# Kernel optimization log

Measured on AMD Instinct MI355X. Metric: run time of the kernel, lower is better.

The kernel has to match this reference:

```python
import jax, jax.numpy as jnp
import numpy as np

# Module hyperparameters (from init_kwargs)
H, F = 8, 32            # num_heads, attention_filters
RY, RX = 3, 3           # spatial_radius
PH, PW = 2 * RY + 1, 2 * RX + 1
S = PH * PW             # patch_size = 49
HF = H * F


def setup_inputs() -> dict:
    key = jax.random.key(0)
    ks = jax.random.split(key, 6)
    B, Y, X, C = 4, 64, 64, 256
    x = jax.random.normal(ks[0], (B, Y, X, C), jnp.float32)
    # 1x1 conv kernels == dense matrices over the channel dim (no bias)
    Wq = jax.random.normal(ks[1], (C, HF), jnp.float32) / np.sqrt(C)
    Wk = jax.random.normal(ks[2], (C, HF), jnp.float32) / np.sqrt(C)
    Wv = jax.random.normal(ks[3], (C, HF), jnp.float32) / np.sqrt(C)
    Wo = jax.random.normal(ks[4], (HF, C), jnp.float32) / np.sqrt(HF)
    pos_emb = jax.random.normal(ks[5], (S, HF), jnp.float32) * 0.02
    return {"x": x, "Wq": Wq, "Wk": Wk, "Wv": Wv, "Wo": Wo, "pos_emb": pos_emb}


def reference(x, Wq, Wk, Wv, Wo, pos_emb):
    B, Y, X, C = x.shape
    dtype = x.dtype
    # 1x1 conv projections
    Q = x @ Wq                       # (B,Y,X,HF)
    K = x @ Wk
    V = x @ Wv
    # clipped patch centers (borders reuse interior patches)
    cy = jnp.clip(jnp.arange(Y), RY, Y - RY - 1)   # (Y,)
    cx = jnp.clip(jnp.arange(X), RX, X - RX - 1)   # (X,)
    # query relative-position indices within its patch
    qy = jnp.arange(Y) - cy + RY
    qx = jnp.arange(X) - cx + RX
    qidx = qy[:, None] * PW + qx[None, :]          # (Y,X) in [0,S)
    Q = Q + pos_emb[qidx]                          # add query pos embedding (HF)
    Q = Q.reshape(B, Y, X, H, F)
    K = K.reshape(B, Y, X, H, F)
    V = V.reshape(B, Y, X, H, F)
    cy_g, cx_g = jnp.meshgrid(cy, cx, indexing="ij")  # (Y,X)
    scale = jnp.asarray(1.0 / np.sqrt(F), dtype)
    NEG = jnp.asarray(-1e9, dtype)
    m = jnp.full((B, Y, X, H, 1), NEG, dtype)      # running max
    l = jnp.zeros((B, Y, X, H, 1), dtype)          # running sum-exp
    acc = jnp.zeros((B, Y, X, H, F), dtype)        # running value accumulator
    dy_vec = np.arange(-RY, RY + 1)                # within-chunk offsets ('col' mode)
    for dx in range(-RX, RX + 1):                  # chunk loop over columns (7 chunks)
        ny = jnp.clip(cy_g[None, :, :] + dy_vec[:, None, None], 0, Y - 1)  # (PH,Y,X)
        nx = jnp.clip(cx_g[None, :, :] + dx, 0, X - 1)                     # (1,Y,X)
        nx = jnp.broadcast_to(nx, ny.shape)
        sidx = (dy_vec + RY) * PW + (dx + RX)      # (PH,) relative-pos indices
        # gather neighbor K/V: (B,PH,Y,X,H,F)
        Kc = K[:, ny, nx] + pos_emb[sidx].reshape(PH, 1, 1, H, F)
        Vc = V[:, ny, nx]
        sc = jnp.einsum("byxhf,bsyxhf->byxhs", Q, Kc) * scale  # (B,Y,X,H,PH)
        new_m = jnp.maximum(m, sc.max(axis=-1, keepdims=True))
        alpha = jnp.exp(m - new_m)
        p = jnp.exp(sc - new_m)
        l = l * alpha + p.sum(axis=-1, keepdims=True)
        acc = acc * alpha + jnp.einsum("byxhs,bsyxhf->byxhf", p, Vc)
        m = new_m
    out = (acc / (l + 1e-8)).reshape(B, Y, X, HF) @ Wo
    return out
```

## Files before the change

### kernel.cpp

```cpp
#include <hip/hip_runtime.h>
#include <hip/hip_bf16.h>

static constexpr int NPOS = 4 * 64 * 64;
static constexpr int CD   = 256;
#define QSCALE (0.17677669529663687f * 1.4426950408889634f)

typedef __attribute__((ext_vector_type(8))) short bf16x8;
typedef __attribute__((ext_vector_type(4))) float f32x4;

__device__ __forceinline__ float bf2f(unsigned short u) {
    return __uint_as_float((unsigned int)u << 16);
}
__device__ __forceinline__ unsigned short bfbits(float f) {
    union { __hip_bfloat16 h; unsigned short u; } cv;
    cv.h = __float2bfloat16(f);
    return cv.u;
}
__device__ __forceinline__ unsigned int packbf2(float lo, float hi) {
    union { __hip_bfloat162 h; unsigned int u; } cv;
    cv.h.x = __float2bfloat16(lo);
    cv.h.y = __float2bfloat16(hi);
    return cv.u;
}
__device__ __forceinline__ uint4 pack8(float4 a, float4 b) {
    uint4 u;
    u.x = packbf2(a.x, a.y); u.y = packbf2(a.z, a.w);
    u.z = packbf2(b.x, b.y); u.w = packbf2(b.z, b.w);
    return u;
}
template<int CTRL>
__device__ __forceinline__ float dpp_mov(float v) {
    return __int_as_float(
        __builtin_amdgcn_update_dpp(0, __float_as_int(v), CTRL, 0xF, 0xF, true));
}
template<int IMM>
__device__ __forceinline__ float swz(float v) {
    return __int_as_float(__builtin_amdgcn_ds_swizzle(__float_as_int(v), IMM));
}

__global__ __launch_bounds__(256) void convert_kernel(
    const float* __restrict__ Wq, const float* __restrict__ Wk,
    const float* __restrict__ Wv, const float* __restrict__ Wo,
    const float* __restrict__ pe,
    __hip_bfloat16* __restrict__ Wfrag,
    __hip_bfloat16* __restrict__ pebf,
    __hip_bfloat16* __restrict__ Wofrag)
{
    int t = blockIdx.x * 256 + threadIdx.x;
    if (t < 24576) {
        int L = t & 63, ng = (t >> 6) & 7, s = (t >> 9) & 7, T = t >> 12;
        int mat = T >> 1;
        const float* src = (mat == 0) ? Wq : (mat == 1) ? Wk : Wv;
        int ncol  = (T & 1) * 128 + ng * 16 + (L & 15);
        int kbase = s * 32 + (L >> 4) * 8;
        __hip_bfloat16* dst = Wfrag + ((size_t)((T * 8 + s) * 8 + ng) * 64 + L) * 8;
#pragma unroll
        for (int j = 0; j < 8; ++j)
            dst[j] = __float2bfloat16(src[(kbase + j) * 256 + ncol]);
    } else if (t < 26624) {
        int u = t - 24576;
        int L = u & 63, Tn = (u >> 6) & 3, h = u >> 8;
        int s = Tn * 16 + (L & 15);
        int kbase = (L >> 4) * 8;
        __hip_bfloat16* dst = pebf + ((size_t)((h * 4 + Tn) * 64 + L)) * 8;
#pragma unroll
        for (int j = 0; j < 8; ++j) {
            float v = (s < 49) ? pe[s * 256 + h * 32 + kbase + j] * QSCALE : 0.f;
            dst[j] = __float2bfloat16(v);
        }
    } else if (t < 34816) {
        int u = t - 26624;
        int L = u & 63, ng = (u >> 6) & 7, s = (u >> 9) & 7, T = (u >> 12) & 1;
        int ncol  = T * 128 + ng * 16 + (L & 15);
        int kbase = s * 32 + (L >> 4) * 8;
        __hip_bfloat16* dst = Wofrag + ((size_t)((T * 8 + s) * 8 + ng) * 64 + L) * 8;
#pragma unroll
        for (int j = 0; j < 8; ++j)
            dst[j] = __float2bfloat16(Wo[(kbase + j) * 256 + ncol]);
    }
}

__global__ __launch_bounds__(256, 4) void qkv_mfma(
    const float* __restrict__ x,
    const __hip_bfloat16* __restrict__ Wfrag,
    const float* __restrict__ pe,
    unsigned short* __restrict__ QA,
    unsigned short* __restrict__ Kd,
    unsigned short* __restrict__ Vt)
{
    __shared__ __align__(16) unsigned short smem[256 * 68];
    short* As0 = (short*)smem;
    short* As1 = As0 + 2048;
    const int t = threadIdx.x;
    const int rowbase = blockIdx.x * 64;
    const int g = blockIdx.y;
    const int L = t & 63;
    const int wave = t >> 6;
    const int quad = L >> 4, lrow = L & 15;
    const int T = g * 2 + (wave >> 1);
    const int ngb = (wave & 1) * 4;

    f32x4 acc[4][4];
#pragma unroll
    for (int i = 0; i < 4; ++i)
#pragma unroll
        for (int j = 0; j < 4; ++j) acc[i][j] = (f32x4){0.f, 0.f, 0.f, 0.f};

    const float* xsrc = x + (size_t)(rowbase + (t >> 2)) * CD + (t & 3) * 8;
    const __hip_bfloat16* wbase = Wfrag + ((size_t)(T * 8 * 8 + ngb) * 64 + L) * 8;

    float4 f0 = ((const float4*)xsrc)[0];
    float4 f1 = ((const float4*)xsrc)[1];
    ((uint4*)As0)[t] = pack8(f0, f1);
    f0 = ((const float4*)(xsrc + 32))[0];
    f1 = ((const float4*)(xsrc + 32))[1];

    bf16x8 bfr[4];
#pragma unroll
    for (int j = 0; j < 4; ++j)
        bfr[j] = *(const bf16x8*)(wbase + (size_t)j * 64 * 8);
    __syncthreads();

#pragma unroll
    for (int s = 0; s < 8; ++s) {
        bf16x8 nbfr[4];
        if (s < 7) {
#pragma unroll
            for (int j = 0; j < 4; ++j)
                nbfr[j] = *(const bf16x8*)(wbase + (size_t)((s + 1) * 8 + j) * 64 * 8);
        }
        if (s < 7) {
            ((uint4*)((s & 1) ? As0 : As1))[t] = pack8(f0, f1);
            if (s < 6) {
                f0 = ((const float4*)(xsrc + (s + 2) * 32))[0];
                f1 = ((const float4*)(xsrc + (s + 2) * 32))[1];
            }
        }
        const short* Ab = (s & 1) ? As1 : As0;
#pragma unroll
        for (int i = 0; i < 4; ++i) {
            bf16x8 af = *(const bf16x8*)(Ab + (i * 16 + lrow) * 32 + quad * 8);
#pragma unroll
            for (int j = 0; j < 4; ++j)
                acc[i][j] = __builtin_amdgcn_mfma_f32_16x16x32_bf16(af, bfr[j], acc[i][j], 0, 0, 0);
        }
        __syncthreads();
#pragma unroll
        for (int j = 0; j < 4; ++j) bfr[j] = nbfr[j];
    }

    if (g == 0) {
#pragma unroll
        for (int i = 0; i < 4; ++i)
#pragma unroll
            for (int r = 0; r < 4; ++r) {
                int row = rowbase + i * 16 + quad * 4 + r;
                int yy = (row >> 6) & 63, xx = row & 63;
                int cy = min(max(yy, 3), 60), cx = min(max(xx, 3), 60);
                int qidx = (yy - cy + 3) * 7 + (xx - cx + 3);
#pragma unroll
                for (int j = 0; j < 4; ++j) {
                    int c = wave * 64 + j * 16 + lrow;
                    QA[(size_t)row * CD + c] = bfbits(acc[i][j][r] + pe[qidx * 256 + c]);
                }
            }
    } else if (g == 1) {
#pragma unroll
        for (int i = 0; i < 4; ++i)
#pragma unroll
            for (int r = 0; r < 4; ++r) {
                int row = rowbase + i * 16 + quad * 4 + r;
#pragma unroll
                for (int j = 0; j < 4; ++j) {
                    int c = wave * 64 + j * 16 + lrow;
                    Kd[(size_t)row * CD + c] = bfbits(acc[i][j][r] * QSCALE);
                }
            }
    } else {
        unsigned short* vt = smem;
#pragma unroll
        for (int i = 0; i < 4; ++i)
#pragma unroll
            for (int j = 0; j < 4; ++j) {
                int c = wave * 64 + j * 16 + lrow;
                int row0 = i * 16 + quad * 4;
                *(unsigned int*)&vt[c * 68 + row0] =
                    (unsigned int)bfbits(acc[i][j][0]) | ((unsigned int)bfbits(acc[i][j][1]) << 16);
                *(unsigned int*)&vt[c * 68 + row0 + 2] =
                    (unsigned int)bfbits(acc[i][j][2]) | ((unsigned int)bfbits(acc[i][j][3]) << 16);
            }
        __syncthreads();
        const int grp = t >> 4, lig = t & 15;
        const int row_off = lig * 4;
#pragma unroll
        for (int pass = 0; pass < 16; ++pass) {
            int c = pass * 16 + grp;
            *(ushort4*)(Vt + (size_t)c * 16384 + rowbase + row_off) =
                *(const ushort4*)&vt[c * 68 + row_off];
        }
    }
}

__global__ __launch_bounds__(512) void attn_oproj(
    const unsigned short* __restrict__ QA,
    const unsigned short* __restrict__ Kd,
    const unsigned short* __restrict__ Vt,
    const __hip_bfloat16* __restrict__ pebf,
    const __hip_bfloat16* __restrict__ Wofrag,
    float* __restrict__ out)
{
    __shared__ unsigned short qpes[8][16 * 64];
    __shared__ __align__(16) unsigned short ps[8][16 * 40];
    __shared__ __align__(16) unsigned short At[16 * 264];
    const int t = threadIdx.x, w = t >> 6, L = t & 63;
    const int lrow = L & 15, quad = L >> 4;
    const int pos0 = blockIdx.x * 16;
    const int x0 = pos0 & 63;
    const int yy = (pos0 >> 6) & 63, bb = pos0 >> 12;
    const int cy = min(max(yy, 3), 60);
    const int h = w;

    int cxr[4];
#pragma unroll
    for (int r = 0; r < 4; ++r)
        cxr[r] = min(max(x0 + quad * 4 + r, 3), 60) - x0 + 5;

    const int kc0 = min(max(x0 - 8 + lrow, 0), 63);
    const int kc1 = min(max(x0 + 8 + lrow, 0), 63);
    const f32x4 zero = {0.f, 0.f, 0.f, 0.f};
    unsigned short* qp = qpes[w];
    unsigned short* pw = ps[w];

    const bf16x8 qa = *(const bf16x8*)(QA + (size_t)(pos0 + lrow) * 256 + h * 32 + quad * 8);

#pragma unroll
    for (int Tn = 0; Tn < 4; ++Tn) {
        bf16x8 bp = *(const bf16x8*)(pebf + ((size_t)((h * 4 + Tn) * 64 + L)) * 8);
        f32x4 c = __builtin_amdgcn_mfma_f32_16x16x32_bf16(qa, bp, zero, 0, 0, 0);
#pragma unroll
        for (int r = 0; r < 4; ++r)
            qp[(quad * 4 + r) * 64 + Tn * 16 + lrow] = bfbits(c[r]);
    }
    __builtin_amdgcn_s_waitcnt(0xc07f);

    float lacc[4] = {0.f, 0.f, 0.f, 0.f};
    f32x4 o0 = zero, o1 = zero;
    int rowpos = bb * 4096 + (cy - 3) * 64;

    const size_t koff = h * 32 + quad * 8;
    const size_t voff0 = (size_t)(h * 32 + lrow) * 16384 + x0 - 8 + quad * 8;
    const size_t voff1 = (size_t)(h * 32 + 16 + lrow) * 16384 + x0 - 8 + quad * 8;
    bf16x8 bk0 = *(const bf16x8*)(Kd + (size_t)(rowpos + kc0) * 256 + koff);
    bf16x8 bk1 = *(const bf16x8*)(Kd + (size_t)(rowpos + kc1) * 256 + koff);
    bf16x8 bv0 = *(const bf16x8*)(Vt + voff0 + rowpos);
    bf16x8 bv1 = *(const bf16x8*)(Vt + voff1 + rowpos);

    for (int dy = 0; dy < 7; ++dy) {
        const int rnext = rowpos + 64;
        bf16x8 nk0, nk1, nv0, nv1;
        if (dy < 6) {
            nk0 = *(const bf16x8*)(Kd + (size_t)(rnext + kc0) * 256 + koff);
            nk1 = *(const bf16x8*)(Kd + (size_t)(rnext + kc1) * 256 + koff);
            nv0 = *(const bf16x8*)(Vt + voff0 + rnext);
            nv1 = *(const bf16x8*)(Vt + voff1 + rnext);
        }
        f32x4 sc0 = __builtin_amdgcn_mfma_f32_16x16x32_bf16(qa, bk0, zero, 0, 0, 0);
        f32x4 sc1 = __builtin_amdgcn_mfma_f32_16x16x32_bf16(qa, bk1, zero, 0, 0, 0);
        const int dy7 = dy * 7;
#pragma unroll
        for (int r = 0; r < 4; ++r) {
            const int i = quad * 4 + r;
            {
                int dx3 = lrow - cxr[r];
                float qpe = bf2f(qp[i * 64 + dy7 + min(max(dx3, 0), 6)]);
                float e = exp2f(sc0[r] + qpe);
                float p = ((unsigned)dx3 <= 6u) ? e : 0.f;
                lacc[r] += p;
                pw[i * 40 + lrow] = bfbits(p);
            }
            {
                int dx3 = 16 + lrow - cxr[r];
                float qpe = bf2f(qp[i * 64 + dy7 + min(max(dx3, 0), 6)]);
                float e = exp2f(sc1[r] + qpe);
                float p = ((unsigned)dx3 <= 6u) ? e : 0.f;
                lacc[r] += p;
                pw[i * 40 + 16 + lrow] = bfbits(p);
            }
        }
        __builtin_amdgcn_s_waitcnt(0xc07f);
        const bf16x8 pa = *(const bf16x8*)(pw + lrow * 40 + quad * 8);
        o0 = __builtin_amdgcn_mfma_f32_16x16x32_bf16(pa, bv0, o0, 0, 0, 0);
        o1 = __builtin_amdgcn_mfma_f32_16x16x32_bf16(pa, bv1, o1, 0, 0, 0);
        bk0 = nk0; bk1 = nk1; bv0 = nv0; bv1 = nv1;
        rowpos = rnext;
    }

#pragma unroll
    for (int r = 0; r < 4; ++r) {
        float v = lacc[r];
        v += dpp_mov<0xB1>(v);
        v += dpp_mov<0x4E>(v);
        v += swz<0x101F>(v);
        v += swz<0x201F>(v);
        const float inv = 1.f / (v + 1e-8f);
        const int arow = quad * 4 + r;
        At[arow * 264 + h * 32 + lrow]      = bfbits(o0[r] * inv);
        At[arow * 264 + h * 32 + 16 + lrow] = bfbits(o1[r] * inv);
    }
    __syncthreads();

    const int T = w >> 2;
    const int ngb = (w & 3) * 2;
    f32x4 acc[2];
    acc[0] = zero; acc[1] = zero;

#pragma unroll
    for (int s = 0; s < 8; ++s) {
        bf16x8 bfr[2];
#pragma unroll
        for (int j = 0; j < 2; ++j)
            bfr[j] = *(const bf16x8*)(Wofrag +
                      ((size_t)((T * 8 + s) * 8 + ngb + j) * 64 + L) * 8);
        bf16x8 af = *(const bf16x8*)(At + lrow * 264 + s * 32 + quad * 8);
#pragma unroll
        for (int j = 0; j < 2; ++j)
            acc[j] = __builtin_amdgcn_mfma_f32_16x16x32_bf16(af, bfr[j], acc[j], 0, 0, 0);
    }

#pragma unroll
    for (int r = 0; r < 4; ++r) {
        int row = pos0 + quad * 4 + r;
#pragma unroll
        for (int j = 0; j < 2; ++j) {
            int c = w * 32 + j * 16 + lrow;
            out[(size_t)row * CD + c] = acc[j][r];
        }
    }
}

extern "C" void kernel_launch(void* const* d_in, const int* in_sizes, int n_in,
                              void* d_out, int out_size, void* d_ws, size_t ws_size,
                              hipStream_t stream)
{
    const float* x  = (const float*)d_in[0];
    const float* Wq = (const float*)d_in[1];
    const float* Wk = (const float*)d_in[2];
    const float* Wv = (const float*)d_in[3];
    const float* Wo = (const float*)d_in[4];
    const float* pe = (const float*)d_in[5];
    float* out = (float*)d_out;

    char* ws = (char*)d_ws;
    unsigned short* QA = (unsigned short*)ws;
    unsigned short* Kd = (unsigned short*)(ws + (8u << 20));
    unsigned short* Vt = (unsigned short*)(ws + (16u << 20));
    char* fr = ws + (24u << 20) + 4096;
    __hip_bfloat16* Wfrag  = (__hip_bfloat16*)fr;
    __hip_bfloat16* pebf   = (__hip_bfloat16*)(fr + (384u << 10));
    __hip_bfloat16* Wofrag = (__hip_bfloat16*)(fr + (416u << 10));

    convert_kernel<<<136, 256, 0, stream>>>(Wq, Wk, Wv, Wo, pe, Wfrag, pebf, Wofrag);
    qkv_mfma<<<dim3(256, 3), 256, 0, stream>>>(x, Wfrag, pe, QA, Kd, Vt);
    attn_oproj<<<1024, 512, 0, stream>>>(QA, Kd, Vt, pebf, Wofrag, out);
}
```

Measured before the change: 124.7 us.

## Software-pipeline attention loop with double-buffered softmax probabilities in LDS

Restructures the per-row attention loop so the P·V MFMAs for row dy-1 are issued alongside the score MFMAs and exp work for row dy. The probability tile is double-buffered in shared memory, and the explicit waitcnt between writing and reading P is removed. Per-lane qpe indices and validity masks are hoisted out of the loop, and masking becomes a multiply instead of a select. The aim is to hide LDS round-trip and MFMA latency, at the cost of more LDS space and a prologue/epilogue peel.

```diff
diff --git a/kernel.cpp b/kernel.cpp
--- a/kernel.cpp
+++ b/kernel.cpp
@@ -210,7 +210,7 @@
     float* __restrict__ out)
 {
     __shared__ unsigned short qpes[8][16 * 64];
-    __shared__ __align__(16) unsigned short ps[8][16 * 40];
+    __shared__ __align__(16) unsigned short ps[8][2][640];
     __shared__ __align__(16) unsigned short At[16 * 264];
     const int t = threadIdx.x, w = t >> 6, L = t & 63;
     const int lrow = L & 15, quad = L >> 4;
@@ -220,16 +220,24 @@
     const int cy = min(max(yy, 3), 60);
     const int h = w;
 
-    int cxr[4];
-#pragma unroll
-    for (int r = 0; r < 4; ++r)
-        cxr[r] = min(max(x0 + quad * 4 + r, 3), 60) - x0 + 5;
-
     const int kc0 = min(max(x0 - 8 + lrow, 0), 63);
     const int kc1 = min(max(x0 + 8 + lrow, 0), 63);
     const f32x4 zero = {0.f, 0.f, 0.f, 0.f};
     unsigned short* qp = qpes[w];
-    unsigned short* pw = ps[w];
+
+    int qi0[4], qi1[4];
+    float mk0[4], mk1[4];
+#pragma unroll
+    for (int r = 0; r < 4; ++r) {
+        const int i = quad * 4 + r;
+        const int cxr = min(max(x0 + i, 3), 60) - x0 + 5;
+        int dx3a = lrow - cxr;
+        qi0[r] = i * 64 + min(max(dx3a, 0), 6);
+        mk0[r] = ((unsigned)dx3a <= 6u) ? 1.f : 0.f;
+        int dx3b = 16 + lrow - cxr;
+        qi1[r] = i * 64 + min(max(dx3b, 0), 6);
+        mk1[r] = ((unsigned)dx3b <= 6u) ? 1.f : 0.f;
+    }
 
     const bf16x8 qa = *(const bf16x8*)(QA + (size_t)(pos0 + lrow) * 256 + h * 32 + quad * 8);
 
@@ -245,54 +253,65 @@
 
     float lacc[4] = {0.f, 0.f, 0.f, 0.f};
     f32x4 o0 = zero, o1 = zero;
-    int rowpos = bb * 4096 + (cy - 3) * 64;
+    const int rowbase0 = bb * 4096 + (cy - 3) * 64;
 
     const size_t koff = h * 32 + quad * 8;
-    const size_t voff0 = (size_t)(h * 32 + lrow) * 16384 + x0 - 8 + quad * 8;
-    const size_t voff1 = (size_t)(h * 32 + 16 + lrow) * 16384 + x0 - 8 + quad * 8;
-    bf16x8 bk0 = *(const bf16x8*)(Kd + (size_t)(rowpos + kc0) * 256 + koff);
-    bf16x8 bk1 = *(const bf16x8*)(Kd + (size_t)(rowpos + kc1) * 256 + koff);
-    bf16x8 bv0 = *(const bf16x8*)(Vt + voff0 + rowpos);
-    bf16x8 bv1 = *(const bf16x8*)(Vt + voff1 + rowpos);
-
-    for (int dy = 0; dy < 7; ++dy) {
-        const int rnext = rowpos + 64;
-        bf16x8 nk0, nk1, nv0, nv1;
+    const unsigned short* Vb0 = Vt + (size_t)(h * 32 + lrow) * 16384 + x0 - 8 + quad * 8;
+    const unsigned short* Vb1 = Vt + (size_t)(h * 32 + 16 + lrow) * 16384 + x0 - 8 + quad * 8;
+    const int pwofs = (quad * 4) * 40 + lrow;
+
+    bf16x8 bk0 = *(const bf16x8*)(Kd + (size_t)(rowbase0 + kc0) * 256 + koff);
+    bf16x8 bk1 = *(const bf16x8*)(Kd + (size_t)(rowbase0 + kc1) * 256 + koff);
+    bf16x8 bv0p = *(const bf16x8*)(Vb0 + rowbase0);
+    bf16x8 bv1p = *(const bf16x8*)(Vb1 + rowbase0);
+    {
+        f32x4 s0 = __builtin_amdgcn_mfma_f32_16x16x32_bf16(qa, bk0, zero, 0, 0, 0);
+        f32x4 s1 = __builtin_amdgcn_mfma_f32_16x16x32_bf16(qa, bk1, zero, 0, 0, 0);
+        bk0 = *(const bf16x8*)(Kd + (size_t)(rowbase0 + 64 + kc0) * 256 + koff);
+        bk1 = *(const bf16x8*)(Kd + (size_t)(rowbase0 + 64 + kc1) * 256 + koff);
+        unsigned short* pwr = &ps[w][0][0];
+#pragma unroll
+        for (int r = 0; r < 4; ++r) {
+            float e0 = exp2f(s0[r] + bf2f(qp[qi0[r]])) * mk0[r];
+            lacc[r] += e0;
+            pwr[pwofs + r * 40] = bfbits(e0);
+            float e1 = exp2f(s1[r] + bf2f(qp[qi1[r]])) * mk1[r];
+            lacc[r] += e1;
+            pwr[pwofs + r * 40 + 16] = bfbits(e1);
+        }
+    }
+
+    int qpofs = 7;
+    for (int dy = 1; dy < 7; ++dy) {
+        const int rp = rowbase0 + dy * 64;
+        bf16x8 bv0n = *(const bf16x8*)(Vb0 + rp);
+        bf16x8 bv1n = *(const bf16x8*)(Vb1 + rp);
+        f32x4 s0 = __builtin_amdgcn_mfma_f32_16x16x32_bf16(qa, bk0, zero, 0, 0, 0);
+        f32x4 s1 = __builtin_amdgcn_mfma_f32_16x16x32_bf16(qa, bk1, zero, 0, 0, 0);
         if (dy < 6) {
-            nk0 = *(const bf16x8*)(Kd + (size_t)(rnext + kc0) * 256 + koff);
-            nk1 = *(const bf16x8*)(Kd + (size_t)(rnext + kc1) * 256 + koff);
-            nv0 = *(const bf16x8*)(Vt + voff0 + rnext);
-            nv1 = *(const bf16x8*)(Vt + voff1 + rnext);
-        }
-        f32x4 sc0 = __builtin_amdgcn_mfma_f32_16x16x32_bf16(qa, bk0, zero, 0, 0, 0);
-        f32x4 sc1 = __builtin_amdgcn_mfma_f32_16x16x32_bf16(qa, bk1, zero, 0, 0, 0);
-        const int dy7 = dy * 7;
+            bk0 = *(const bf16x8*)(Kd + (size_t)(rp + 64 + kc0) * 256 + koff);
+            bk1 = *(const bf16x8*)(Kd + (size_t)(rp + 64 + kc1) * 256 + koff);
+        }
+        const bf16x8 pa = *(const bf16x8*)(&ps[w][(dy - 1) & 1][0] + lrow * 40 + quad * 8);
+        o0 = __builtin_amdgcn_mfma_f32_16x16x32_bf16(pa, bv0p, o0, 0, 0, 0);
+        o1 = __builtin_amdgcn_mfma_f32_16x16x32_bf16(pa, bv1p, o1, 0, 0, 0);
+        unsigned short* pwr = &ps[w][dy & 1][0];
 #pragma unroll
         for (int r = 0; r < 4; ++r) {
-            const int i = quad * 4 + r;
-            {
-                int dx3 = lrow - cxr[r];
-                float qpe = bf2f(qp[i * 64 + dy7 + min(max(dx3, 0), 6)]);
-                float e = exp2f(sc0[r] + qpe);
-                float p = ((unsigned)dx3 <= 6u) ? e : 0.f;
-                lacc[r] += p;
-                pw[i * 40 + lrow] = bfbits(p);
-            }
-            {
-                int dx3 = 16 + lrow - cxr[r];
-                float qpe = bf2f(qp[i * 64 + dy7 + min(max(dx3, 0), 6)]);
-                float e = exp2f(sc1[r] + qpe);
-                float p = ((unsigned)dx3 <= 6u) ? e : 0.f;
-                lacc[r] += p;
-                pw[i * 40 + 16 + lrow] = bfbits(p);
-            }
-        }
-        __builtin_amdgcn_s_waitcnt(0xc07f);
-        const bf16x8 pa = *(const bf16x8*)(pw + lrow * 40 + quad * 8);
-        o0 = __builtin_amdgcn_mfma_f32_16x16x32_bf16(pa, bv0, o0, 0, 0, 0);
-        o1 = __builtin_amdgcn_mfma_f32_16x16x32_bf16(pa, bv1, o1, 0, 0, 0);
-        bk0 = nk0; bk1 = nk1; bv0 = nv0; bv1 = nv1;
-        rowpos = rnext;
+            float e0 = exp2f(s0[r] + bf2f(qp[qi0[r] + qpofs])) * mk0[r];
+            lacc[r] += e0;
+            pwr[pwofs + r * 40] = bfbits(e0);
+            float e1 = exp2f(s1[r] + bf2f(qp[qi1[r] + qpofs])) * mk1[r];
+            lacc[r] += e1;
+            pwr[pwofs + r * 40 + 16] = bfbits(e1);
+        }
+        qpofs += 7;
+        bv0p = bv0n; bv1p = bv1n;
+    }
+    {
+        const bf16x8 pa = *(const bf16x8*)(&ps[w][0][0] + lrow * 40 + quad * 8);
+        o0 = __builtin_amdgcn_mfma_f32_16x16x32_bf16(pa, bv0p, o0, 0, 0, 0);
+        o1 = __builtin_amdgcn_mfma_f32_16x16x32_bf16(pa, bv1p, o1, 0, 0, 0);
     }
 
 #pragma unroll
```

Measured after the change: 130.0 us. +4.2%, slower.
